# Optimization experiments

Hardware: AMD Instinct MI355X
Metric: run time of the kernel (lower is better)

Reference implementation:

```python
import jax, jax.numpy as jnp
import numpy as np

B, H, W = 16, 512, 512


def conv2d(x, w, b):
    # NCHW conv, stride 1, padding 1 (SAME for 3x3)
    y = jax.lax.conv_general_dilated(
        x, w, window_strides=(1, 1), padding=((1, 1), (1, 1)),
        dimension_numbers=("NCHW", "OIHW", "NCHW"))
    return y + b[None, :, None, None]


def bilinear_sample(img, py, px):
    # img: [B,H,W]; py,px: [B,K,H,W] float sample coords. Zero padding outside.
    Hh, Ww = img.shape[1], img.shape[2]
    y0 = jnp.floor(py)
    x0 = jnp.floor(px)
    wy = py - y0  # fractional weights
    wx = px - x0
    y0i = y0.astype(jnp.int32)
    x0i = x0.astype(jnp.int32)

    def gather(yi, xi):
        valid = (yi >= 0) & (yi < Hh) & (xi >= 0) & (xi < Ww)
        yc = jnp.clip(yi, 0, Hh - 1)
        xc = jnp.clip(xi, 0, Ww - 1)
        v = jax.vmap(lambda im, yy, xx: im[yy, xx])(img, yc, xc)
        return jnp.where(valid, v, jnp.zeros((), img.dtype))

    v00 = gather(y0i, x0i)
    v01 = gather(y0i, x0i + 1)
    v10 = gather(y0i + 1, x0i)
    v11 = gather(y0i + 1, x0i + 1)
    return (v00 * (1 - wy) * (1 - wx) + v01 * (1 - wy) * wx
            + v10 * wy * (1 - wx) + v11 * wy * wx)


def setup_inputs() -> dict:
    key = jax.random.key(0)
    ks = jax.random.split(key, 7)
    pm25 = jax.random.normal(ks[0], (B, 1, H, W), jnp.float32)
    avg_wind = jax.random.normal(ks[1], (B, 2, H, W), jnp.float32)
    topo = jax.random.normal(ks[2], (B, 1, H, W), jnp.float32)
    # offset_conv params (Kaiming-ish small random)
    conv1_w = jax.random.normal(ks[3], (16, 3, 3, 3), jnp.float32) * (1.0 / np.sqrt(3 * 9))
    conv1_b = jax.random.normal(ks[4], (16,), jnp.float32) * 0.01
    conv2_w = jax.random.normal(ks[5], (18, 16, 3, 3), jnp.float32) * (1.0 / np.sqrt(16 * 9))
    conv2_b = jax.random.normal(ks[6], (18,), jnp.float32) * 0.01
    # dirac init: identity 3x3 kernel
    weight = jnp.zeros((1, 1, 3, 3), jnp.float32).at[0, 0, 1, 1].set(1.0)
    return {"pm25": pm25, "avg_wind": avg_wind, "topo": topo,
            "conv1_w": conv1_w, "conv1_b": conv1_b,
            "conv2_w": conv2_w, "conv2_b": conv2_b, "weight": weight}


def reference(pm25, avg_wind, topo, conv1_w, conv1_b, conv2_w, conv2_b, weight):
    # offset-predicting conv stack
    feat = jax.nn.gelu(conv2d(jnp.concatenate([avg_wind, topo], axis=1), conv1_w, conv1_b), approximate=False)
    offsets = conv2d(feat, conv2_w, conv2_b)          # [B, 2*3*3, H, W]
    b, _, h, w = offsets.shape
    off = offsets.reshape(b, 9, 2, h, w)              # k = i*3 + j; [.,k,0]=dy, [.,k,1]=dx
    dy, dx = off[:, :, 0], off[:, :, 1]               # [B,9,H,W]

    ys = jnp.arange(h, dtype=pm25.dtype)[None, None, :, None]
    xs = jnp.arange(w, dtype=pm25.dtype)[None, None, None, :]
    ki = jnp.arange(3, dtype=pm25.dtype)
    kdy = (jnp.repeat(ki, 3) - 1.0)[None, :, None, None]  # kernel row offset - pad
    kdx = (jnp.tile(ki, 3) - 1.0)[None, :, None, None]    # kernel col offset - pad

    py = ys + kdy + dy                                # sample rows   [B,9,H,W]
    px = xs + kdx + dx                                # sample cols   [B,9,H,W]

    samp = bilinear_sample(pm25[:, 0], py, px)        # [B,9,H,W]
    wk = weight.reshape(9)                            # single-channel 3x3 kernel
    out = jnp.einsum("bkhw,k->bhw", samp, wk)[:, None]
    return out                                        # [B,1,H,W]
```

## Files before the change

kernel.cpp:

```cpp
#include <hip/hip_runtime.h>
#include <math.h>

#define Bn 16
#define Hh 512
#define Ww 512
#define HW_ (Hh * Ww)
#define TILE 32
#define NTHREADS 1024
#define S 37
#define SIN_N 1400
#define NFP 1280
#define NT2 80

typedef __bf16 bfrag __attribute__((ext_vector_type(8)));
typedef __bf16 bf4   __attribute__((ext_vector_type(4)));
typedef float  ffrag __attribute__((ext_vector_type(16)));
typedef float  f32x4 __attribute__((ext_vector_type(4)));
typedef float  f32x2 __attribute__((ext_vector_type(2)));

__device__ __forceinline__ short f2bf(float f) {
    unsigned u = __float_as_uint(f);
    unsigned r = u + 0x7FFFu + ((u >> 16) & 1u);
    return (short)(r >> 16);
}

__device__ __forceinline__ f32x2 mk2(float a, float b) { f32x2 t; t.x = a; t.y = b; return t; }

__device__ __forceinline__ f32x2 gelu_fast2(f32x2 x) {
    const float C0 = 1.1259890f, C1 = -0.3565430f, C2 = 0.0848830f,
                C3 = -0.0110610f, C4 = 0.0005820f;
    f32x2 y = x * 0.70710678f;
    f32x2 t;
    t.x = fminf(fmaxf(y.x, -2.5f), 2.5f);
    t.y = fminf(fmaxf(y.y, -2.5f), 2.5f);
    f32x2 u = t * t;
    f32x2 p = u * C4 + C3;
    p = p * u + C2;
    p = p * u + C1;
    p = p * u + C0;
    f32x2 e = t * p;
    f32x2 h = x * 0.5f;
    return h * e + h;
}

__device__ __forceinline__ float bilin(const float* __restrict__ img, float py, float px) {
    float y0f = floorf(py), x0f = floorf(px);
    float wy = py - y0f, wx = px - x0f;
    int y0 = (int)y0f, x0 = (int)x0f;
    int yc0 = min(max(y0, 0), Hh - 1), yc1 = min(max(y0 + 1, 0), Hh - 1);
    int xc0 = min(max(x0, 0), Ww - 1), xc1 = min(max(x0 + 1, 0), Ww - 1);
    bool vy0 = (unsigned)y0 < (unsigned)Hh, vy1 = (unsigned)(y0 + 1) < (unsigned)Hh;
    bool vx0 = (unsigned)x0 < (unsigned)Ww, vx1 = (unsigned)(x0 + 1) < (unsigned)Ww;
    const float* r0 = img + yc0 * Ww;
    const float* r1 = img + yc1 * Ww;
    float v00 = (vy0 && vx0) ? r0[xc0] : 0.0f;
    float v01 = (vy0 && vx1) ? r0[xc1] : 0.0f;
    float v10 = (vy1 && vx0) ? r1[xc0] : 0.0f;
    float v11 = (vy1 && vx1) ? r1[xc1] : 0.0f;
    return (1.0f - wy) * ((1.0f - wx) * v00 + wx * v01) +
           wy          * ((1.0f - wx) * v10 + wx * v11);
}

__global__ void pack_w(const float* __restrict__ w2, const float* __restrict__ w1,
                       const float* __restrict__ b1, int* __restrict__ ws) {
    const int lane = threadIdx.x;
    const int l31  = lane & 31;
    const int lh   = lane >> 5;
    for (int tap = 0; tap < 9; ++tap) {
        int pk[4];
        #pragma unroll
        for (int jj = 0; jj < 4; ++jj) {
            float v0 = (l31 < 18) ? w2[(l31 * 16 + lh * 8 + 2 * jj    ) * 9 + tap] : 0.0f;
            float v1 = (l31 < 18) ? w2[(l31 * 16 + lh * 8 + 2 * jj + 1) * 9 + tap] : 0.0f;
            pk[jj] = ((int)(unsigned short)f2bf(v0)) | ((int)f2bf(v1) << 16);
        }
        ((int4*)ws)[tap * 64 + lane] = make_int4(pk[0], pk[1], pk[2], pk[3]);
    }
    const int m  = lane & 15;
    const int kq = lane >> 4;
    for (int t = 0; t < 2; ++t) {
        int pk[4];
        #pragma unroll
        for (int jj = 0; jj < 4; ++jj) {
            float vv[2];
            #pragma unroll
            for (int h = 0; h < 2; ++h) {
                int k   = kq * 8 + 2 * jj + h;
                int kyl = k >> 4, kx = (k >> 2) & 3, c = k & 3;
                int ky  = 2 * t + kyl;
                float x = 0.0f;
                if (kx < 3 && c < 3 && ky < 3) x = w1[m * 27 + c * 9 + ky * 3 + kx];
                if (t == 0 && k == 3) x = b1[m];
                vv[h] = x;
            }
            pk[jj] = ((int)(unsigned short)f2bf(vv[0])) | ((int)f2bf(vv[1]) << 16);
        }
        ((int4*)ws)[576 + t * 64 + lane] = make_int4(pk[0], pk[1], pk[2], pk[3]);
    }
}

#define SMEM_BYTES (SIN_N * 16 + 2 * NFP * 16)

__global__ __launch_bounds__(NTHREADS, 8) void residual_advection_fused(
    const float* __restrict__ pm25,
    const float* __restrict__ wind,
    const float* __restrict__ topo,
    const float* __restrict__ b2,
    const float* __restrict__ wt,
    const int*   __restrict__ wsB,
    float* __restrict__ out)
{
    __shared__ __align__(16) char smem[SMEM_BYTES];
    __bf16* s_in   = (__bf16*)smem;
    __bf16* s_feat = (__bf16*)(smem + SIN_N * 16);

    const int tid = threadIdx.x;
    const int bb  = blockIdx.z;
    const int ty0 = blockIdx.y * TILE;
    const int tx0 = blockIdx.x * TILE;
    const bool edge = (ty0 == 0) || (ty0 == Hh - TILE) || (tx0 == 0) || (tx0 == Ww - TILE);

    const int lane = tid & 63;
    const int wv   = tid >> 6;
    const int l31  = lane & 31;
    const int lh   = lane >> 5;

    const bfrag* WF = (const bfrag*)wsB;

    bfrag w1f0 = WF[576 + lane];
    bfrag w1f1 = WF[640 + lane];

    for (int idx = tid; idx < SIN_N; idx += NTHREADS) {
        float c0 = 0.0f, c1 = 0.0f, c2 = 0.0f;
        if (idx < 36 * S) {
            int r = idx / S, c = idx - r * S;
            if (!edge) {
                int g = (ty0 - 2 + r) * Ww + (tx0 - 2 + c);
                c0 = wind[(bb * 2 + 0) * HW_ + g];
                c1 = wind[(bb * 2 + 1) * HW_ + g];
                c2 = topo[bb * HW_ + g];
            } else {
                int gy = ty0 - 2 + r, gx = tx0 - 2 + c;
                if ((unsigned)gy < (unsigned)Hh && (unsigned)gx < (unsigned)Ww) {
                    int g = gy * Ww + gx;
                    c0 = wind[(bb * 2 + 0) * HW_ + g];
                    c1 = wind[(bb * 2 + 1) * HW_ + g];
                    c2 = topo[bb * HW_ + g];
                }
            }
        }
        bf4 v;
        v[0] = (__bf16)c0; v[1] = (__bf16)c1; v[2] = (__bf16)c2; v[3] = (__bf16)1.0f;
        *(bf4*)&s_in[idx * 8] = v;
        if (idx > 0) *(bf4*)&s_in[idx * 8 - 4] = v;
    }
    __syncthreads();

    {
        const int n    = lane & 15;
        const int kq   = lane >> 4;
        const int qoff = (kq >> 1) * S + (kq & 1) * 2;
        #pragma unroll
        for (int i = 0; i < 5; ++i) {
            const int p = (wv * 5 + i) * 16 + n;
            f32x4 acc;
            acc[0] = 0.0f; acc[1] = 0.0f; acc[2] = 0.0f; acc[3] = 0.0f;
            bfrag bx0 = *(const bfrag*)&s_in[(p + qoff) * 8];
            bfrag bx1 = *(const bfrag*)&s_in[(p + qoff + 2 * S) * 8];
            acc = __builtin_amdgcn_mfma_f32_16x16x32_bf16(w1f0, bx0, acc, 0, 0, 0);
            acc = __builtin_amdgcn_mfma_f32_16x16x32_bf16(w1f1, bx1, acc, 0, 0, 0);
            f32x2 g0 = gelu_fast2(mk2(acc[0], acc[1]));
            f32x2 g1 = gelu_fast2(mk2(acc[2], acc[3]));
            if (edge) {
                int fy = p / S;
                int fx = p - fy * S;
                int gy = ty0 + fy - 1, gx = tx0 + fx - 1;
                float msk = ((unsigned)gy < (unsigned)Hh && (unsigned)gx < (unsigned)Ww)
                            ? 1.0f : 0.0f;
                g0 *= msk; g1 *= msk;
            }
            bf4 w4;
            w4[0] = (__bf16)g0.x; w4[1] = (__bf16)g0.y;
            w4[2] = (__bf16)g1.x; w4[3] = (__bf16)g1.y;
            *(bf4*)&s_feat[((kq >> 1) * NFP + p) * 8 + (kq & 1) * 4] = w4;
        }
    }
    __syncthreads();

    ffrag a0, a1;
    #pragma unroll
    for (int r = 0; r < 16; ++r) { a0[r] = 0.0f; a1[r] = 0.0f; }
    {
        const int vb = (lh * NFP + (2 * wv) * S + l31) * 8;
        #pragma unroll
        for (int kx = 0; kx < 3; ++kx) {
            bfrag f0 = *(const bfrag*)&s_feat[vb + (0 * S + kx) * 8];
            bfrag f1 = *(const bfrag*)&s_feat[vb + (1 * S + kx) * 8];
            bfrag f2 = *(const bfrag*)&s_feat[vb + (2 * S + kx) * 8];
            bfrag f3 = *(const bfrag*)&s_feat[vb + (3 * S + kx) * 8];
            bfrag w0 = WF[(0 * 3 + kx) * 64 + lane];
            bfrag w1_ = WF[(1 * 3 + kx) * 64 + lane];
            bfrag w2_ = WF[(2 * 3 + kx) * 64 + lane];
            a0 = __builtin_amdgcn_mfma_f32_32x32x16_bf16(w0,  f0, a0, 0, 0, 0);
            a1 = __builtin_amdgcn_mfma_f32_32x32x16_bf16(w0,  f1, a1, 0, 0, 0);
            a0 = __builtin_amdgcn_mfma_f32_32x32x16_bf16(w1_, f1, a0, 0, 0, 0);
            a1 = __builtin_amdgcn_mfma_f32_32x32x16_bf16(w1_, f2, a1, 0, 0, 0);
            a0 = __builtin_amdgcn_mfma_f32_32x32x16_bf16(w2_, f2, a0, 0, 0, 0);
            a1 = __builtin_amdgcn_mfma_f32_32x32x16_bf16(w2_, f3, a1, 0, 0, 0);
        }
    }

    {
        const float* img = pm25 + bb * HW_;
        const int py_i = ty0 + 2 * wv + lh;
        const int px_i = tx0 + l31;
        const float fy = (float)py_i, fx = (float)px_i;
        float o = 0.0f;
        #pragma unroll
        for (int t = 0; t < 9; ++t) {
            float wk = wt[t];
            if (wk != 0.0f) {
                const int o_h = (t >> 1) & 1;
                const int rg  = ((2 * t) & 3) + 4 * (t >> 2);
                float dy, dx;
                if (o_h == 0) {
                    float sy = __shfl_xor(a1[rg], 32);
                    float sx = __shfl_xor(a1[rg + 1], 32);
                    dy = lh ? sy : a0[rg];
                    dx = lh ? sx : a0[rg + 1];
                } else {
                    float sy = __shfl_xor(a0[rg], 32);
                    float sx = __shfl_xor(a0[rg + 1], 32);
                    dy = lh ? a1[rg] : sy;
                    dx = lh ? a1[rg + 1] : sx;
                }
                dy += b2[2 * t];
                dx += b2[2 * t + 1];
                float py = fy + (float)(t / 3 - 1) + dy;
                float px = fx + (float)(t % 3 - 1) + dx;
                o += wk * bilin(img, py, px);
            }
        }
        out[bb * HW_ + py_i * Ww + px_i] = o;
    }
}

extern "C" void kernel_launch(void* const* d_in, const int* in_sizes, int n_in,
                              void* d_out, int out_size, void* d_ws, size_t ws_size,
                              hipStream_t stream) {
    const float* pm25 = (const float*)d_in[0];
    const float* wind = (const float*)d_in[1];
    const float* topo = (const float*)d_in[2];
    const float* w1   = (const float*)d_in[3];
    const float* b1   = (const float*)d_in[4];
    const float* w2   = (const float*)d_in[5];
    const float* b2   = (const float*)d_in[6];
    const float* wt   = (const float*)d_in[7];
    float* o          = (float*)d_out;
    int*   wsB        = (int*)d_ws;

    pack_w<<<dim3(1), dim3(64), 0, stream>>>(w2, w1, b1, wsB);

    dim3 grid(Ww / TILE, Hh / TILE, Bn);
    residual_advection_fused<<<grid, dim3(NTHREADS), 0, stream>>>(
        pm25, wind, topo, b2, wt, wsB, o);
}
```

Baseline: 176.8 us.

## Give each wavefront a private halo tile to drop block-wide barriers

Replaces the 1024-thread block, which shared a 32x32 tile with two __syncthreads, with 256-thread blocks in which each wavefront independently computes a 2x32 output strip using its own private LDS region. Each wave loads its own 6x36 input halo and computes 4x36 features, so no cross-wave synchronization is needed. The cost is much more redundant halo loading and conv1 recomputation per output pixel (roughly 3x the conv1 work), in exchange for removing barrier stalls and allowing finer-grained scheduling.

```diff
diff --git a/kernel.cpp b/kernel.cpp
--- a/kernel.cpp
+++ b/kernel.cpp
@@ -5,12 +5,15 @@
 #define Hh 512
 #define Ww 512
 #define HW_ (Hh * Ww)
-#define TILE 32
-#define NTHREADS 1024
-#define S 37
-#define SIN_N 1400
-#define NFP 1280
-#define NT2 80
+#define TW 32
+#define WROWS 2
+#define WPB 4
+#define NTHREADS 256
+#define SI 36
+#define SIN_E 256
+#define NFE 144
+#define WAVE_LDS (SIN_E * 16 + 2 * NFE * 16)
+#define SMEM_BYTES (WPB * WAVE_LDS)
 
 typedef __bf16 bfrag __attribute__((ext_vector_type(8)));
 typedef __bf16 bf4   __attribute__((ext_vector_type(4)));
@@ -99,9 +102,7 @@
     }
 }
 
-#define SMEM_BYTES (SIN_N * 16 + 2 * NFP * 16)
-
-__global__ __launch_bounds__(NTHREADS, 8) void residual_advection_fused(
+__global__ __launch_bounds__(NTHREADS, 4) void residual_advection_fused(
     const float* __restrict__ pm25,
     const float* __restrict__ wind,
     const float* __restrict__ topo,
@@ -111,70 +112,68 @@
     float* __restrict__ out)
 {
     __shared__ __align__(16) char smem[SMEM_BYTES];
-    __bf16* s_in   = (__bf16*)smem;
-    __bf16* s_feat = (__bf16*)(smem + SIN_N * 16);
-
-    const int tid = threadIdx.x;
-    const int bb  = blockIdx.z;
-    const int ty0 = blockIdx.y * TILE;
-    const int tx0 = blockIdx.x * TILE;
-    const bool edge = (ty0 == 0) || (ty0 == Hh - TILE) || (tx0 == 0) || (tx0 == Ww - TILE);
-
+
+    const int tid  = threadIdx.x;
     const int lane = tid & 63;
     const int wv   = tid >> 6;
     const int l31  = lane & 31;
     const int lh   = lane >> 5;
 
+    const int bb = blockIdx.z;
+    const int x0 = blockIdx.x * TW;
+    const int yb = blockIdx.y * (WPB * WROWS) + 2 * wv;
+
+    __bf16* s_in   = (__bf16*)(smem + wv * WAVE_LDS);
+    __bf16* s_feat = (__bf16*)(smem + wv * WAVE_LDS + SIN_E * 16);
+
     const bfrag* WF = (const bfrag*)wsB;
-
     bfrag w1f0 = WF[576 + lane];
     bfrag w1f1 = WF[640 + lane];
 
-    for (int idx = tid; idx < SIN_N; idx += NTHREADS) {
+    const float* wp0 = wind + (bb * 2 + 0) * HW_;
+    const float* wp1 = wind + (bb * 2 + 1) * HW_;
+    const float* tp  = topo + bb * HW_;
+    const float* img = pm25 + bb * HW_;
+
+    const bool edge = (yb < 2) || (yb > Hh - 4) || (x0 == 0) || (x0 == Ww - TW);
+
+    #pragma unroll
+    for (int k = 0; k < 4; ++k) {
+        const int p = lane + 64 * k;
+        const int r = p / SI, c = p - r * SI;
         float c0 = 0.0f, c1 = 0.0f, c2 = 0.0f;
-        if (idx < 36 * S) {
-            int r = idx / S, c = idx - r * S;
-            if (!edge) {
-                int g = (ty0 - 2 + r) * Ww + (tx0 - 2 + c);
-                c0 = wind[(bb * 2 + 0) * HW_ + g];
-                c1 = wind[(bb * 2 + 1) * HW_ + g];
-                c2 = topo[bb * HW_ + g];
-            } else {
-                int gy = ty0 - 2 + r, gx = tx0 - 2 + c;
-                if ((unsigned)gy < (unsigned)Hh && (unsigned)gx < (unsigned)Ww) {
-                    int g = gy * Ww + gx;
-                    c0 = wind[(bb * 2 + 0) * HW_ + g];
-                    c1 = wind[(bb * 2 + 1) * HW_ + g];
-                    c2 = topo[bb * HW_ + g];
-                }
+        if (r < 6) {
+            int gy = yb - 2 + r, gx = x0 - 2 + c;
+            if (!edge || ((unsigned)gy < (unsigned)Hh && (unsigned)gx < (unsigned)Ww)) {
+                int g = gy * Ww + gx;
+                c0 = wp0[g]; c1 = wp1[g]; c2 = tp[g];
             }
         }
         bf4 v;
         v[0] = (__bf16)c0; v[1] = (__bf16)c1; v[2] = (__bf16)c2; v[3] = (__bf16)1.0f;
-        *(bf4*)&s_in[idx * 8] = v;
-        if (idx > 0) *(bf4*)&s_in[idx * 8 - 4] = v;
-    }
-    __syncthreads();
+        *(bf4*)&s_in[p * 8] = v;
+        if (p > 0) *(bf4*)&s_in[p * 8 - 4] = v;
+    }
 
     {
         const int n    = lane & 15;
         const int kq   = lane >> 4;
-        const int qoff = (kq >> 1) * S + (kq & 1) * 2;
-        #pragma unroll
-        for (int i = 0; i < 5; ++i) {
-            const int p = (wv * 5 + i) * 16 + n;
+        const int qoff = (kq >> 1) * SI + (kq & 1) * 2;
+        #pragma unroll 3
+        for (int t = 0; t < 9; ++t) {
+            const int p = t * 16 + n;
             f32x4 acc;
             acc[0] = 0.0f; acc[1] = 0.0f; acc[2] = 0.0f; acc[3] = 0.0f;
             bfrag bx0 = *(const bfrag*)&s_in[(p + qoff) * 8];
-            bfrag bx1 = *(const bfrag*)&s_in[(p + qoff + 2 * S) * 8];
+            bfrag bx1 = *(const bfrag*)&s_in[(p + qoff + 2 * SI) * 8];
             acc = __builtin_amdgcn_mfma_f32_16x16x32_bf16(w1f0, bx0, acc, 0, 0, 0);
             acc = __builtin_amdgcn_mfma_f32_16x16x32_bf16(w1f1, bx1, acc, 0, 0, 0);
             f32x2 g0 = gelu_fast2(mk2(acc[0], acc[1]));
             f32x2 g1 = gelu_fast2(mk2(acc[2], acc[3]));
             if (edge) {
-                int fy = p / S;
-                int fx = p - fy * S;
-                int gy = ty0 + fy - 1, gx = tx0 + fx - 1;
+                int fy = p / SI;
+                int fx = p - fy * SI;
+                int gy = yb - 1 + fy, gx = x0 - 1 + fx;
                 float msk = ((unsigned)gy < (unsigned)Hh && (unsigned)gx < (unsigned)Ww)
                             ? 1.0f : 0.0f;
                 g0 *= msk; g1 *= msk;
@@ -182,23 +181,22 @@
             bf4 w4;
             w4[0] = (__bf16)g0.x; w4[1] = (__bf16)g0.y;
             w4[2] = (__bf16)g1.x; w4[3] = (__bf16)g1.y;
-            *(bf4*)&s_feat[((kq >> 1) * NFP + p) * 8 + (kq & 1) * 4] = w4;
-        }
-    }
-    __syncthreads();
+            *(bf4*)&s_feat[((kq >> 1) * NFE + p) * 8 + (kq & 1) * 4] = w4;
+        }
+    }
 
     ffrag a0, a1;
     #pragma unroll
     for (int r = 0; r < 16; ++r) { a0[r] = 0.0f; a1[r] = 0.0f; }
     {
-        const int vb = (lh * NFP + (2 * wv) * S + l31) * 8;
+        const int vb = (lh * NFE + l31) * 8;
         #pragma unroll
         for (int kx = 0; kx < 3; ++kx) {
-            bfrag f0 = *(const bfrag*)&s_feat[vb + (0 * S + kx) * 8];
-            bfrag f1 = *(const bfrag*)&s_feat[vb + (1 * S + kx) * 8];
-            bfrag f2 = *(const bfrag*)&s_feat[vb + (2 * S + kx) * 8];
-            bfrag f3 = *(const bfrag*)&s_feat[vb + (3 * S + kx) * 8];
-            bfrag w0 = WF[(0 * 3 + kx) * 64 + lane];
+            bfrag f0 = *(const bfrag*)&s_feat[vb + (0 * SI + kx) * 8];
+            bfrag f1 = *(const bfrag*)&s_feat[vb + (1 * SI + kx) * 8];
+            bfrag f2 = *(const bfrag*)&s_feat[vb + (2 * SI + kx) * 8];
+            bfrag f3 = *(const bfrag*)&s_feat[vb + (3 * SI + kx) * 8];
+            bfrag w0  = WF[(0 * 3 + kx) * 64 + lane];
             bfrag w1_ = WF[(1 * 3 + kx) * 64 + lane];
             bfrag w2_ = WF[(2 * 3 + kx) * 64 + lane];
             a0 = __builtin_amdgcn_mfma_f32_32x32x16_bf16(w0,  f0, a0, 0, 0, 0);
@@ -211,9 +209,8 @@
     }
 
     {
-        const float* img = pm25 + bb * HW_;
-        const int py_i = ty0 + 2 * wv + lh;
-        const int px_i = tx0 + l31;
+        const int py_i = yb + lh;
+        const int px_i = x0 + l31;
         const float fy = (float)py_i, fx = (float)px_i;
         float o = 0.0f;
         #pragma unroll
@@ -261,7 +258,7 @@
 
     pack_w<<<dim3(1), dim3(64), 0, stream>>>(w2, w1, b1, wsB);
 
-    dim3 grid(Ww / TILE, Hh / TILE, Bn);
+    dim3 grid(Ww / TW, Hh / (WPB * WROWS), Bn);
     residual_advection_fused<<<grid, dim3(NTHREADS), 0, stream>>>(
         pm25, wind, topo, b2, wt, wsB, o);
 }
```

New measurement: 219.4 us. +24.1%, slower.
